# Kernel tuning notes

Measured on AMD Instinct MI355X. Metric: run time of the kernel, lower is better.

Reference implementation:

```python
import jax, jax.numpy as jnp
import numpy as np

KERNEL_SIZE = 5   # from __init__ default
SIGMA_S = 1.0     # spatial gaussian sigma (both axes)
SIGMA_R = 0.04    # range (color) gaussian sigma


def _space_kernel(k, sigma):
    # kornia-style 1D gaussian, normalized to sum 1, then outer product -> (k, k)
    x = jnp.arange(k, dtype=jnp.float32) - (k // 2)
    g = jnp.exp(-(x * x) / (2.0 * sigma * sigma))
    g = g / g.sum()
    return jnp.outer(g, g)


def setup_inputs() -> dict:
    key = jax.random.key(0)
    images = jax.random.uniform(key, (16, 512, 512, 3), dtype=jnp.float32)  # [B,H,W,3] in [0,1]
    return {"images": images}


def reference(images):
    k = KERNEL_SIZE
    pad = k // 2
    x = jnp.transpose(images, (0, 3, 1, 2))  # (B, C, H, W)
    B, C, H, W = x.shape
    xp = jnp.pad(x, ((0, 0), (0, 0), (pad, pad), (pad, pad)), mode="reflect")
    sk = _space_kernel(k, SIGMA_S).astype(x.dtype)
    inv2sr2 = 0.5 / (SIGMA_R * SIGMA_R)
    num = jnp.zeros_like(x)
    den = jnp.zeros((B, 1, H, W), dtype=x.dtype)
    # fused accumulation over the k*k window (fixed 25-tap loop, fully vectorized per tap)
    for dy in range(k):
        for dx in range(k):
            sh = xp[:, :, dy:dy + H, dx:dx + W]                  # shifted neighbor (B,C,H,W)
            d2 = jnp.sum((sh - x) ** 2, axis=1, keepdims=True)   # color distance^2 (B,1,H,W)
            w = sk[dy, dx] * jnp.exp(-inv2sr2 * d2)              # space * range weight
            num = num + w * sh
            den = den + w
    out = jnp.clip(num / den, 0.0, 1.0)
    return jnp.transpose(out, (0, 2, 3, 1))  # back to (B, H, W, C)
```

## Files before the change

### kernel.cpp

```cpp
#include <hip/hip_runtime.h>
#include <hip/hip_fp16.h>
#include <math.h>

#define IMG_H 512
#define IMG_W 512
#define CH    3
#define TILE_W 16
#define TILE_H 64
#define QTR   16
#define PAD   2
#define TP    20

#if __has_builtin(__builtin_amdgcn_rcpf)
#define RCP(x) __builtin_amdgcn_rcpf(x)
#else
#define RCP(x) (1.0f / (x))
#endif

__device__ __forceinline__ int reflect_idx(int i, int n) {
    i = (i < 0) ? -i : i;
    i = (i >= n) ? (2 * n - 2 - i) : i;
    return i;
}

__device__ __forceinline__ __half2 bch(unsigned int u) {
    return __builtin_bit_cast(__half2, u);
}
__device__ __forceinline__ unsigned int hcb(__half2 h) {
    return __builtin_bit_cast(unsigned int, h);
}

__global__ __launch_bounds__(256)
void bilateral_kernel(const float* __restrict__ in, float* __restrict__ out) {
    __shared__ uint4 H4[TP][TP];
    __shared__ uint2 H2[TP][TP];

    const int b  = blockIdx.z;
    const int by = blockIdx.y * TILE_H;
    const int bx = blockIdx.x * TILE_W;
    const int tx = threadIdx.x;
    const int ty = threadIdx.y;
    const int tid = ty * TILE_W + tx;

    for (int i = tid; i < TP * TP; i += 256) {
        const int r  = i / TP;
        const int cc = i - r * TP;
        const int gx  = reflect_idx(bx + cc - PAD, IMG_W);
        const int gyA = reflect_idx(by + r - PAD, IMG_H);
        const int gyB = reflect_idx(by + QTR + r - PAD, IMG_H);
        const int gyC = reflect_idx(by + 2 * QTR + r - PAD, IMG_H);
        const int gyD = reflect_idx(by + 3 * QTR + r - PAD, IMG_H);
        const float* pA = in + ((size_t)(b * IMG_H + gyA) * IMG_W + gx) * CH;
        const float* pB = in + ((size_t)(b * IMG_H + gyB) * IMG_W + gx) * CH;
        const float* pC = in + ((size_t)(b * IMG_H + gyC) * IMG_W + gx) * CH;
        const float* pD = in + ((size_t)(b * IMG_H + gyD) * IMG_W + gx) * CH;
        uint4 h4;
        uint2 h2;
        h4.x = hcb(__floats2half2_rn(pA[0], pB[0]));
        h4.y = hcb(__floats2half2_rn(pC[0], pD[0]));
        h4.z = hcb(__floats2half2_rn(pA[1], pB[1]));
        h4.w = hcb(__floats2half2_rn(pC[1], pD[1]));
        h2.x = hcb(__floats2half2_rn(pA[2], pB[2]));
        h2.y = hcb(__floats2half2_rn(pC[2], pD[2]));
        H4[r][cc] = h4;
        H2[r][cc] = h2;
    }
    __syncthreads();

    const int rp = ((ty & 3) << 2) | (ty >> 2);

    const __half2 K2 = __float2half2_rn(-450.8422f);
    const __half2 B2[3][3] = {
        { __float2half2_rn(-8.395800f), __float2half2_rn(-6.231757f), __float2half2_rn(-5.510409f) },
        { __float2half2_rn(-6.231757f), __float2half2_rn(-4.067714f), __float2half2_rn(-3.346367f) },
        { __float2half2_rn(-5.510409f), __float2half2_rn(-3.346367f), __float2half2_rn(-2.625024f) },
    };

    const uint4 cP = H4[rp + PAD][tx + PAD];
    const uint2 cQ = H2[rp + PAD][tx + PAD];
    const __half2 cxAB = bch(cP.x), cxCD = bch(cP.y);
    const __half2 cyAB = bch(cP.z), cyCD = bch(cP.w);
    const __half2 czAB = bch(cQ.x), czCD = bch(cQ.y);

    const __half2 z2 = __float2half2_rn(0.0f);
    __half2 nxAB = z2, nyAB = z2, nzAB = z2, ndAB = z2;
    __half2 nxCD = z2, nyCD = z2, nzCD = z2, ndCD = z2;

    #pragma unroll
    for (int dy = 0; dy < 5; ++dy) {
        const int iy = (dy < 3) ? dy : 4 - dy;
        #pragma unroll
        for (int k = 0; k < 5; ++k) {
            const int ix = (k < 3) ? k : 4 - k;
            const uint4 P = H4[rp + dy][tx + k];
            const uint2 Q = H2[rp + dy][tx + k];
            const __half2 sxAB = bch(P.x), sxCD = bch(P.y);
            const __half2 syAB = bch(P.z), syCD = bch(P.w);
            const __half2 szAB = bch(Q.x), szCD = bch(Q.y);
            {
                const __half2 dx = __hsub2(sxAB, cxAB);
                const __half2 dyh = __hsub2(syAB, cyAB);
                const __half2 dz = __hsub2(szAB, czAB);
                const __half2 d2 = __hfma2(dx, dx, __hfma2(dyh, dyh, __hmul2(dz, dz)));
                const __half2 arg = __hfma2(d2, K2, B2[iy][ix]);
                const __half2 w = h2exp2(arg);
                nxAB = __hfma2(w, sxAB, nxAB);
                nyAB = __hfma2(w, syAB, nyAB);
                nzAB = __hfma2(w, szAB, nzAB);
                ndAB = __hadd2(ndAB, w);
            }
            {
                const __half2 dx = __hsub2(sxCD, cxCD);
                const __half2 dyh = __hsub2(syCD, cyCD);
                const __half2 dz = __hsub2(szCD, czCD);
                const __half2 d2 = __hfma2(dx, dx, __hfma2(dyh, dyh, __hmul2(dz, dz)));
                const __half2 arg = __hfma2(d2, K2, B2[iy][ix]);
                const __half2 w = h2exp2(arg);
                nxCD = __hfma2(w, sxCD, nxCD);
                nyCD = __hfma2(w, syCD, nyCD);
                nzCD = __hfma2(w, szCD, nzCD);
                ndCD = __hadd2(ndCD, w);
            }
        }
    }

    const int xcol = bx + tx;
    #pragma unroll
    for (int q = 0; q < 4; ++q) {
        float n0, n1, n2, den;
        if (q == 0) { n0 = __low2float(nxAB);  n1 = __low2float(nyAB);  n2 = __low2float(nzAB);  den = __low2float(ndAB); }
        else if (q == 1) { n0 = __high2float(nxAB); n1 = __high2float(nyAB); n2 = __high2float(nzAB); den = __high2float(ndAB); }
        else if (q == 2) { n0 = __low2float(nxCD);  n1 = __low2float(nyCD);  n2 = __low2float(nzCD);  den = __low2float(ndCD); }
        else { n0 = __high2float(nxCD); n1 = __high2float(nyCD); n2 = __high2float(nzCD); den = __high2float(ndCD); }
        const float inv = RCP(den);
        const int y = by + q * QTR + rp;
        float* dst = out + ((size_t)(b * IMG_H + y) * IMG_W + xcol) * CH;
        dst[0] = fminf(fmaxf(n0 * inv, 0.0f), 1.0f);
        dst[1] = fminf(fmaxf(n1 * inv, 0.0f), 1.0f);
        dst[2] = fminf(fmaxf(n2 * inv, 0.0f), 1.0f);
    }
}

extern "C" void kernel_launch(void* const* d_in, const int* in_sizes, int n_in,
                              void* d_out, int out_size, void* d_ws, size_t ws_size,
                              hipStream_t stream) {
    const float* in = (const float*)d_in[0];
    float* out = (float*)d_out;
    const int B = in_sizes[0] / (IMG_H * IMG_W * CH);

    dim3 block(TILE_W, 16, 1);
    dim3 grid(IMG_W / TILE_W, IMG_H / TILE_H, B);
    bilateral_kernel<<<grid, block, 0, stream>>>(in, out);
}
```

Before: 39.22 us.

## Process two vertical tiles per block with double-buffered LDS prefetch

Each block now handles two stacked 64-row tiles. It double-buffers the shared-memory halo and issues the global loads for the next tile while the current tile's tap rows compute. This hides global load latency behind compute and halves the grid size. The cost is more registers for the staged values and an extra sync per tile, plus less parallelism in the grid (512 blocks per batch dimension becomes 256).

```diff
diff --git a/kernel.cpp b/kernel.cpp
--- a/kernel.cpp
+++ b/kernel.cpp
@@ -7,6 +7,7 @@
 #define CH    3
 #define TILE_W 16
 #define TILE_H 64
+#define NT    2
 #define QTR   16
 #define PAD   2
 #define TP    20
@@ -32,39 +33,48 @@
 
 __global__ __launch_bounds__(256)
 void bilateral_kernel(const float* __restrict__ in, float* __restrict__ out) {
-    __shared__ uint4 H4[TP][TP];
-    __shared__ uint2 H2[TP][TP];
+    __shared__ uint4 H4[NT][TP][TP];
+    __shared__ uint2 H2[NT][TP][TP];
 
-    const int b  = blockIdx.z;
-    const int by = blockIdx.y * TILE_H;
-    const int bx = blockIdx.x * TILE_W;
-    const int tx = threadIdx.x;
-    const int ty = threadIdx.y;
+    const int b   = blockIdx.z;
+    const int by0 = blockIdx.y * (TILE_H * NT);
+    const int bx  = blockIdx.x * TILE_W;
+    const int tx  = threadIdx.x;
+    const int ty  = threadIdx.y;
     const int tid = ty * TILE_W + tx;
 
-    for (int i = tid; i < TP * TP; i += 256) {
-        const int r  = i / TP;
-        const int cc = i - r * TP;
-        const int gx  = reflect_idx(bx + cc - PAD, IMG_W);
-        const int gyA = reflect_idx(by + r - PAD, IMG_H);
-        const int gyB = reflect_idx(by + QTR + r - PAD, IMG_H);
-        const int gyC = reflect_idx(by + 2 * QTR + r - PAD, IMG_H);
-        const int gyD = reflect_idx(by + 3 * QTR + r - PAD, IMG_H);
-        const float* pA = in + ((size_t)(b * IMG_H + gyA) * IMG_W + gx) * CH;
-        const float* pB = in + ((size_t)(b * IMG_H + gyB) * IMG_W + gx) * CH;
-        const float* pC = in + ((size_t)(b * IMG_H + gyC) * IMG_W + gx) * CH;
-        const float* pD = in + ((size_t)(b * IMG_H + gyD) * IMG_W + gx) * CH;
-        uint4 h4;
-        uint2 h2;
-        h4.x = hcb(__floats2half2_rn(pA[0], pB[0]));
-        h4.y = hcb(__floats2half2_rn(pC[0], pD[0]));
-        h4.z = hcb(__floats2half2_rn(pA[1], pB[1]));
-        h4.w = hcb(__floats2half2_rn(pC[1], pD[1]));
-        h2.x = hcb(__floats2half2_rn(pA[2], pB[2]));
-        h2.y = hcb(__floats2half2_rn(pC[2], pD[2]));
-        H4[r][cc] = h4;
-        H2[r][cc] = h2;
-    }
+    const int i1  = tid + 256;
+    const int r0e = tid / TP, c0e = tid - r0e * TP;
+    const int r1e = i1  / TP, c1e = i1  - r1e * TP;
+    const bool a1 = (i1 < TP * TP);
+    const int gx0 = reflect_idx(bx + c0e - PAD, IMG_W);
+    const int gx1 = reflect_idx(bx + c1e - PAD, IMG_W);
+
+    float s0v[12], s1v[12];
+
+#define ISSUE(t, re, gx, act, dst)                                           \
+    do { _Pragma("unroll")                                                   \
+        for (int q = 0; q < 4; ++q) {                                        \
+            const int gy = reflect_idx(by0 + (t) * TILE_H + q * QTR + (re) - PAD, IMG_H); \
+            const float* p = in + ((size_t)(b * IMG_H + gy) * IMG_W + (gx)) * CH; \
+            if (act) { (dst)[q*3+0] = p[0]; (dst)[q*3+1] = p[1]; (dst)[q*3+2] = p[2]; } \
+        } } while (0)
+
+#define STORE_LDS(t, re, ce, act, src)                                       \
+    do { if (act) {                                                          \
+        uint4 h4; uint2 h2;                                                  \
+        h4.x = hcb(__floats2half2_rn((src)[0], (src)[3]));                   \
+        h4.y = hcb(__floats2half2_rn((src)[6], (src)[9]));                   \
+        h4.z = hcb(__floats2half2_rn((src)[1], (src)[4]));                   \
+        h4.w = hcb(__floats2half2_rn((src)[7], (src)[10]));                  \
+        h2.x = hcb(__floats2half2_rn((src)[2], (src)[5]));                   \
+        h2.y = hcb(__floats2half2_rn((src)[8], (src)[11]));                  \
+        H4[(t) & 1][re][ce] = h4; H2[(t) & 1][re][ce] = h2; } } while (0)
+
+    ISSUE(0, r0e, gx0, true, s0v);
+    ISSUE(0, r1e, gx1, a1, s1v);
+    STORE_LDS(0, r0e, c0e, true, s0v);
+    STORE_LDS(0, r1e, c1e, a1, s1v);
     __syncthreads();
 
     const int rp = ((ty & 3) << 2) | (ty >> 2);
@@ -76,68 +86,76 @@
         { __float2half2_rn(-5.510409f), __float2half2_rn(-3.346367f), __float2half2_rn(-2.625024f) },
     };
 
-    const uint4 cP = H4[rp + PAD][tx + PAD];
-    const uint2 cQ = H2[rp + PAD][tx + PAD];
-    const __half2 cxAB = bch(cP.x), cxCD = bch(cP.y);
-    const __half2 cyAB = bch(cP.z), cyCD = bch(cP.w);
-    const __half2 czAB = bch(cQ.x), czCD = bch(cQ.y);
+    #pragma unroll
+    for (int t = 0; t < NT; ++t) {
+        const uint4 cP = H4[t & 1][rp + PAD][tx + PAD];
+        const uint2 cQ = H2[t & 1][rp + PAD][tx + PAD];
+        const __half2 cxAB = bch(cP.x), cxCD = bch(cP.y);
+        const __half2 cyAB = bch(cP.z), cyCD = bch(cP.w);
+        const __half2 czAB = bch(cQ.x), czCD = bch(cQ.y);
 
-    const __half2 z2 = __float2half2_rn(0.0f);
-    __half2 nxAB = z2, nyAB = z2, nzAB = z2, ndAB = z2;
-    __half2 nxCD = z2, nyCD = z2, nzCD = z2, ndCD = z2;
+        const __half2 z2 = __float2half2_rn(0.0f);
+        __half2 nxAB = z2, nyAB = z2, nzAB = z2, ndAB = z2;
+        __half2 nxCD = z2, nyCD = z2, nzCD = z2, ndCD = z2;
 
-    #pragma unroll
-    for (int dy = 0; dy < 5; ++dy) {
-        const int iy = (dy < 3) ? dy : 4 - dy;
+#define TAPROW(dy)                                                           \
+        { const int iy = ((dy) < 3) ? (dy) : 4 - (dy);                       \
+          _Pragma("unroll")                                                  \
+          for (int k = 0; k < 5; ++k) {                                      \
+            const int ix = (k < 3) ? k : 4 - k;                              \
+            const uint4 P = H4[t & 1][rp + (dy)][tx + k];                    \
+            const uint2 Q = H2[t & 1][rp + (dy)][tx + k];                    \
+            const __half2 sxAB = bch(P.x), sxCD = bch(P.y);                  \
+            const __half2 syAB = bch(P.z), syCD = bch(P.w);                  \
+            const __half2 szAB = bch(Q.x), szCD = bch(Q.y);                  \
+            {                                                                \
+                const __half2 dx = __hsub2(sxAB, cxAB);                      \
+                const __half2 dh = __hsub2(syAB, cyAB);                      \
+                const __half2 dz = __hsub2(szAB, czAB);                      \
+                const __half2 d2 = __hfma2(dx, dx, __hfma2(dh, dh, __hmul2(dz, dz))); \
+                const __half2 w = h2exp2(__hfma2(d2, K2, B2[iy][ix]));       \
+                nxAB = __hfma2(w, sxAB, nxAB);                               \
+                nyAB = __hfma2(w, syAB, nyAB);                               \
+                nzAB = __hfma2(w, szAB, nzAB);                               \
+                ndAB = __hadd2(ndAB, w);                                     \
+            }                                                                \
+            {                                                                \
+                const __half2 dx = __hsub2(sxCD, cxCD);                      \
+                const __half2 dh = __hsub2(syCD, cyCD);                      \
+                const __half2 dz = __hsub2(szCD, czCD);                      \
+                const __half2 d2 = __hfma2(dx, dx, __hfma2(dh, dh, __hmul2(dz, dz))); \
+                const __half2 w = h2exp2(__hfma2(d2, K2, B2[iy][ix]));       \
+                nxCD = __hfma2(w, sxCD, nxCD);                               \
+                nyCD = __hfma2(w, syCD, nyCD);                               \
+                nzCD = __hfma2(w, szCD, nzCD);                               \
+                ndCD = __hadd2(ndCD, w);                                     \
+            }                                                                \
+          } }
+
+        if (t + 1 < NT) ISSUE(t + 1, r0e, gx0, true, s0v);
+        TAPROW(0) TAPROW(1) TAPROW(2)
+        if (t + 1 < NT) { STORE_LDS(t + 1, r0e, c0e, true, s0v); ISSUE(t + 1, r1e, gx1, a1, s1v); }
+        TAPROW(3) TAPROW(4)
+        if (t + 1 < NT) STORE_LDS(t + 1, r1e, c1e, a1, s1v);
+#undef TAPROW
+
+        const int xcol = bx + tx;
         #pragma unroll
-        for (int k = 0; k < 5; ++k) {
-            const int ix = (k < 3) ? k : 4 - k;
-            const uint4 P = H4[rp + dy][tx + k];
-            const uint2 Q = H2[rp + dy][tx + k];
-            const __half2 sxAB = bch(P.x), sxCD = bch(P.y);
-            const __half2 syAB = bch(P.z), syCD = bch(P.w);
-            const __half2 szAB = bch(Q.x), szCD = bch(Q.y);
-            {
-                const __half2 dx = __hsub2(sxAB, cxAB);
-                const __half2 dyh = __hsub2(syAB, cyAB);
-                const __half2 dz = __hsub2(szAB, czAB);
-                const __half2 d2 = __hfma2(dx, dx, __hfma2(dyh, dyh, __hmul2(dz, dz)));
-                const __half2 arg = __hfma2(d2, K2, B2[iy][ix]);
-                const __half2 w = h2exp2(arg);
-                nxAB = __hfma2(w, sxAB, nxAB);
-                nyAB = __hfma2(w, syAB, nyAB);
-                nzAB = __hfma2(w, szAB, nzAB);
-                ndAB = __hadd2(ndAB, w);
-            }
-            {
-                const __half2 dx = __hsub2(sxCD, cxCD);
-                const __half2 dyh = __hsub2(syCD, cyCD);
-                const __half2 dz = __hsub2(szCD, czCD);
-                const __half2 d2 = __hfma2(dx, dx, __hfma2(dyh, dyh, __hmul2(dz, dz)));
-                const __half2 arg = __hfma2(d2, K2, B2[iy][ix]);
-                const __half2 w = h2exp2(arg);
-                nxCD = __hfma2(w, sxCD, nxCD);
-                nyCD = __hfma2(w, syCD, nyCD);
-                nzCD = __hfma2(w, szCD, nzCD);
-                ndCD = __hadd2(ndCD, w);
-            }
+        for (int q = 0; q < 4; ++q) {
+            float n0, n1, n2, den;
+            if (q == 0)      { n0 = __low2float(nxAB);  n1 = __low2float(nyAB);  n2 = __low2float(nzAB);  den = __low2float(ndAB); }
+            else if (q == 1) { n0 = __high2float(nxAB); n1 = __high2float(nyAB); n2 = __high2float(nzAB); den = __high2float(ndAB); }
+            else if (q == 2) { n0 = __low2float(nxCD);  n1 = __low2float(nyCD);  n2 = __low2float(nzCD);  den = __low2float(ndCD); }
+            else             { n0 = __high2float(nxCD); n1 = __high2float(nyCD); n2 = __high2float(nzCD); den = __high2float(ndCD); }
+            const float inv = RCP(den);
+            const int y = by0 + t * TILE_H + q * QTR + rp;
+            float* dst = out + ((size_t)(b * IMG_H + y) * IMG_W + xcol) * CH;
+            dst[0] = fminf(fmaxf(n0 * inv, 0.0f), 1.0f);
+            dst[1] = fminf(fmaxf(n1 * inv, 0.0f), 1.0f);
+            dst[2] = fminf(fmaxf(n2 * inv, 0.0f), 1.0f);
         }
-    }
 
-    const int xcol = bx + tx;
-    #pragma unroll
-    for (int q = 0; q < 4; ++q) {
-        float n0, n1, n2, den;
-        if (q == 0) { n0 = __low2float(nxAB);  n1 = __low2float(nyAB);  n2 = __low2float(nzAB);  den = __low2float(ndAB); }
-        else if (q == 1) { n0 = __high2float(nxAB); n1 = __high2float(nyAB); n2 = __high2float(nzAB); den = __high2float(ndAB); }
-        else if (q == 2) { n0 = __low2float(nxCD);  n1 = __low2float(nyCD);  n2 = __low2float(nzCD);  den = __low2float(ndCD); }
-        else { n0 = __high2float(nxCD); n1 = __high2float(nyCD); n2 = __high2float(nzCD); den = __high2float(ndCD); }
-        const float inv = RCP(den);
-        const int y = by + q * QTR + rp;
-        float* dst = out + ((size_t)(b * IMG_H + y) * IMG_W + xcol) * CH;
-        dst[0] = fminf(fmaxf(n0 * inv, 0.0f), 1.0f);
-        dst[1] = fminf(fmaxf(n1 * inv, 0.0f), 1.0f);
-        dst[2] = fminf(fmaxf(n2 * inv, 0.0f), 1.0f);
+        __syncthreads();
     }
 }
 
@@ -149,6 +167,6 @@
     const int B = in_sizes[0] / (IMG_H * IMG_W * CH);
 
     dim3 block(TILE_W, 16, 1);
-    dim3 grid(IMG_W / TILE_W, IMG_H / TILE_H, B);
+    dim3 grid(IMG_W / TILE_W, IMG_H / (TILE_H * NT), B);
     bilateral_kernel<<<grid, block, 0, stream>>>(in, out);
 }
```

Result: slower. 42.89 us (+9.3%).

## Pack eight row strips per thread into shared tiles for more work per block

Applied to the files above, without the earlier changes.

Doubles the tile height so each thread filters 8 output rows (four half2 pairs) instead of 4, with one packed uint4 shared array per channel. This halves the number of blocks and spreads the per-block index math, sync and shared loads across twice as many pixels. The cost is more registers per thread (16 half2 accumulators plus centers), fewer blocks available to fill the GPU (1024 instead of 2048), and a longer serial load phase per block.

```diff
diff --git a/kernel.cpp b/kernel.cpp
--- a/kernel.cpp
+++ b/kernel.cpp
@@ -6,8 +6,9 @@
 #define IMG_W 512
 #define CH    3
 #define TILE_W 16
-#define TILE_H 64
+#define TILE_H 128
 #define QTR   16
+#define NQ    8
 #define PAD   2
 #define TP    20
 
@@ -32,8 +33,9 @@
 
 __global__ __launch_bounds__(256)
 void bilateral_kernel(const float* __restrict__ in, float* __restrict__ out) {
-    __shared__ uint4 H4[TP][TP];
-    __shared__ uint2 H2[TP][TP];
+    __shared__ uint4 HX[TP][TP];
+    __shared__ uint4 HY[TP][TP];
+    __shared__ uint4 HZ[TP][TP];
 
     const int b  = blockIdx.z;
     const int by = blockIdx.y * TILE_H;
@@ -45,25 +47,28 @@
     for (int i = tid; i < TP * TP; i += 256) {
         const int r  = i / TP;
         const int cc = i - r * TP;
-        const int gx  = reflect_idx(bx + cc - PAD, IMG_W);
-        const int gyA = reflect_idx(by + r - PAD, IMG_H);
-        const int gyB = reflect_idx(by + QTR + r - PAD, IMG_H);
-        const int gyC = reflect_idx(by + 2 * QTR + r - PAD, IMG_H);
-        const int gyD = reflect_idx(by + 3 * QTR + r - PAD, IMG_H);
-        const float* pA = in + ((size_t)(b * IMG_H + gyA) * IMG_W + gx) * CH;
-        const float* pB = in + ((size_t)(b * IMG_H + gyB) * IMG_W + gx) * CH;
-        const float* pC = in + ((size_t)(b * IMG_H + gyC) * IMG_W + gx) * CH;
-        const float* pD = in + ((size_t)(b * IMG_H + gyD) * IMG_W + gx) * CH;
-        uint4 h4;
-        uint2 h2;
-        h4.x = hcb(__floats2half2_rn(pA[0], pB[0]));
-        h4.y = hcb(__floats2half2_rn(pC[0], pD[0]));
-        h4.z = hcb(__floats2half2_rn(pA[1], pB[1]));
-        h4.w = hcb(__floats2half2_rn(pC[1], pD[1]));
-        h2.x = hcb(__floats2half2_rn(pA[2], pB[2]));
-        h2.y = hcb(__floats2half2_rn(pC[2], pD[2]));
-        H4[r][cc] = h4;
-        H2[r][cc] = h2;
+        const int gx = reflect_idx(bx + cc - PAD, IMG_W);
+        float xs[NQ], ys[NQ], zs[NQ];
+        #pragma unroll
+        for (int q = 0; q < NQ; ++q) {
+            const int gy = reflect_idx(by + q * QTR + r - PAD, IMG_H);
+            const float* p = in + ((size_t)(b * IMG_H + gy) * IMG_W + gx) * CH;
+            xs[q] = p[0]; ys[q] = p[1]; zs[q] = p[2];
+        }
+        uint4 hx, hy, hz;
+        hx.x = hcb(__floats2half2_rn(xs[0], xs[1]));
+        hx.y = hcb(__floats2half2_rn(xs[2], xs[3]));
+        hx.z = hcb(__floats2half2_rn(xs[4], xs[5]));
+        hx.w = hcb(__floats2half2_rn(xs[6], xs[7]));
+        hy.x = hcb(__floats2half2_rn(ys[0], ys[1]));
+        hy.y = hcb(__floats2half2_rn(ys[2], ys[3]));
+        hy.z = hcb(__floats2half2_rn(ys[4], ys[5]));
+        hy.w = hcb(__floats2half2_rn(ys[6], ys[7]));
+        hz.x = hcb(__floats2half2_rn(zs[0], zs[1]));
+        hz.y = hcb(__floats2half2_rn(zs[2], zs[3]));
+        hz.z = hcb(__floats2half2_rn(zs[4], zs[5]));
+        hz.w = hcb(__floats2half2_rn(zs[6], zs[7]));
+        HX[r][cc] = hx; HY[r][cc] = hy; HZ[r][cc] = hz;
     }
     __syncthreads();
 
@@ -76,15 +81,29 @@
         { __float2half2_rn(-5.510409f), __float2half2_rn(-3.346367f), __float2half2_rn(-2.625024f) },
     };
 
-    const uint4 cP = H4[rp + PAD][tx + PAD];
-    const uint2 cQ = H2[rp + PAD][tx + PAD];
-    const __half2 cxAB = bch(cP.x), cxCD = bch(cP.y);
-    const __half2 cyAB = bch(cP.z), cyCD = bch(cP.w);
-    const __half2 czAB = bch(cQ.x), czCD = bch(cQ.y);
+    const uint4 cX = HX[rp + PAD][tx + PAD];
+    const uint4 cY = HY[rp + PAD][tx + PAD];
+    const uint4 cZ = HZ[rp + PAD][tx + PAD];
 
     const __half2 z2 = __float2half2_rn(0.0f);
-    __half2 nxAB = z2, nyAB = z2, nzAB = z2, ndAB = z2;
-    __half2 nxCD = z2, nyCD = z2, nzCD = z2, ndCD = z2;
+    __half2 nx0 = z2, ny0 = z2, nz0 = z2, nd0 = z2;
+    __half2 nx1 = z2, ny1 = z2, nz1 = z2, nd1 = z2;
+    __half2 nx2 = z2, ny2 = z2, nz2 = z2, nd2 = z2;
+    __half2 nx3 = z2, ny3 = z2, nz3 = z2, nd3 = z2;
+
+#define STREAM(comp, cXc, cYc, cZc, nx, ny, nz, nd)                          \
+    {                                                                        \
+        const __half2 sx = bch(P.comp), sy = bch(Y.comp), sz = bch(Z.comp);  \
+        const __half2 dx = __hsub2(sx, bch(cXc));                            \
+        const __half2 dh = __hsub2(sy, bch(cYc));                            \
+        const __half2 dz = __hsub2(sz, bch(cZc));                            \
+        const __half2 d2 = __hfma2(dx, dx, __hfma2(dh, dh, __hmul2(dz, dz))); \
+        const __half2 w = h2exp2(__hfma2(d2, K2, Bv));                       \
+        nx = __hfma2(w, sx, nx);                                             \
+        ny = __hfma2(w, sy, ny);                                             \
+        nz = __hfma2(w, sz, nz);                                             \
+        nd = __hadd2(nd, w);                                                 \
+    }
 
     #pragma unroll
     for (int dy = 0; dy < 5; ++dy) {
@@ -92,53 +111,41 @@
         #pragma unroll
         for (int k = 0; k < 5; ++k) {
             const int ix = (k < 3) ? k : 4 - k;
-            const uint4 P = H4[rp + dy][tx + k];
-            const uint2 Q = H2[rp + dy][tx + k];
-            const __half2 sxAB = bch(P.x), sxCD = bch(P.y);
-            const __half2 syAB = bch(P.z), syCD = bch(P.w);
-            const __half2 szAB = bch(Q.x), szCD = bch(Q.y);
-            {
-                const __half2 dx = __hsub2(sxAB, cxAB);
-                const __half2 dyh = __hsub2(syAB, cyAB);
-                const __half2 dz = __hsub2(szAB, czAB);
-                const __half2 d2 = __hfma2(dx, dx, __hfma2(dyh, dyh, __hmul2(dz, dz)));
-                const __half2 arg = __hfma2(d2, K2, B2[iy][ix]);
-                const __half2 w = h2exp2(arg);
-                nxAB = __hfma2(w, sxAB, nxAB);
-                nyAB = __hfma2(w, syAB, nyAB);
-                nzAB = __hfma2(w, szAB, nzAB);
-                ndAB = __hadd2(ndAB, w);
-            }
-            {
-                const __half2 dx = __hsub2(sxCD, cxCD);
-                const __half2 dyh = __hsub2(syCD, cyCD);
-                const __half2 dz = __hsub2(szCD, czCD);
-                const __half2 d2 = __hfma2(dx, dx, __hfma2(dyh, dyh, __hmul2(dz, dz)));
-                const __half2 arg = __hfma2(d2, K2, B2[iy][ix]);
-                const __half2 w = h2exp2(arg);
-                nxCD = __hfma2(w, sxCD, nxCD);
-                nyCD = __hfma2(w, syCD, nyCD);
-                nzCD = __hfma2(w, szCD, nzCD);
-                ndCD = __hadd2(ndCD, w);
-            }
+            const uint4 P = HX[rp + dy][tx + k];
+            const uint4 Y = HY[rp + dy][tx + k];
+            const uint4 Z = HZ[rp + dy][tx + k];
+            const __half2 Bv = B2[iy][ix];
+            STREAM(x, cX.x, cY.x, cZ.x, nx0, ny0, nz0, nd0)
+            STREAM(y, cX.y, cY.y, cZ.y, nx1, ny1, nz1, nd1)
+            STREAM(z, cX.z, cY.z, cZ.z, nx2, ny2, nz2, nd2)
+            STREAM(w, cX.w, cY.w, cZ.w, nx3, ny3, nz3, nd3)
         }
     }
+#undef STREAM
 
     const int xcol = bx + tx;
-    #pragma unroll
-    for (int q = 0; q < 4; ++q) {
-        float n0, n1, n2, den;
-        if (q == 0) { n0 = __low2float(nxAB);  n1 = __low2float(nyAB);  n2 = __low2float(nzAB);  den = __low2float(ndAB); }
-        else if (q == 1) { n0 = __high2float(nxAB); n1 = __high2float(nyAB); n2 = __high2float(nzAB); den = __high2float(ndAB); }
-        else if (q == 2) { n0 = __low2float(nxCD);  n1 = __low2float(nyCD);  n2 = __low2float(nzCD);  den = __low2float(ndCD); }
-        else { n0 = __high2float(nxCD); n1 = __high2float(nyCD); n2 = __high2float(nzCD); den = __high2float(ndCD); }
-        const float inv = RCP(den);
-        const int y = by + q * QTR + rp;
-        float* dst = out + ((size_t)(b * IMG_H + y) * IMG_W + xcol) * CH;
-        dst[0] = fminf(fmaxf(n0 * inv, 0.0f), 1.0f);
-        dst[1] = fminf(fmaxf(n1 * inv, 0.0f), 1.0f);
-        dst[2] = fminf(fmaxf(n2 * inv, 0.0f), 1.0f);
+#define EMIT(q, nx, ny, nz, nd, SEL_LO)                                      \
+    {                                                                        \
+        const float n0 = SEL_LO ? __low2float(nx) : __high2float(nx);        \
+        const float n1 = SEL_LO ? __low2float(ny) : __high2float(ny);        \
+        const float n2 = SEL_LO ? __low2float(nz) : __high2float(nz);        \
+        const float dn = SEL_LO ? __low2float(nd) : __high2float(nd);        \
+        const float inv = RCP(dn);                                           \
+        const int y = by + (q) * QTR + rp;                                   \
+        float* dst = out + ((size_t)(b * IMG_H + y) * IMG_W + xcol) * CH;    \
+        dst[0] = fminf(fmaxf(n0 * inv, 0.0f), 1.0f);                         \
+        dst[1] = fminf(fmaxf(n1 * inv, 0.0f), 1.0f);                         \
+        dst[2] = fminf(fmaxf(n2 * inv, 0.0f), 1.0f);                         \
     }
+    EMIT(0, nx0, ny0, nz0, nd0, 1)
+    EMIT(1, nx0, ny0, nz0, nd0, 0)
+    EMIT(2, nx1, ny1, nz1, nd1, 1)
+    EMIT(3, nx1, ny1, nz1, nd1, 0)
+    EMIT(4, nx2, ny2, nz2, nd2, 1)
+    EMIT(5, nx2, ny2, nz2, nd2, 0)
+    EMIT(6, nx3, ny3, nz3, nd3, 1)
+    EMIT(7, nx3, ny3, nz3, nd3, 0)
+#undef EMIT
 }
 
 extern "C" void kernel_launch(void* const* d_in, const int* in_sizes, int n_in,
```

New measurement: 40.19 us. 2.5% more time.
